# Optimization experiments

Measured on AMD Instinct MI355X. Metric: run time of the kernel, lower is better.

## Reference

```python
import jax, jax.numpy as jnp
import numpy as np

N = 131072          # number of depos
W = 10              # static raster window (cells per dim); covers 2*nsigma*sigma_max/spacing
NSIGMA = 3.0
SQRT2 = 1.4142135623730951


def setup_inputs() -> dict:
    key = jax.random.key(0)
    k1, k2, k3, k4 = jax.random.split(key, 4)
    # Gaussian widths in [0.25, 0.75] (distance units) so +-3 sigma fits in W=10 cells of 0.5
    sigma = 0.25 + 0.5 * jax.random.uniform(k1, (N, 3), dtype=jnp.float32)
    time = 100.0 * jax.random.uniform(k2, (N,), dtype=jnp.float32)
    charge = 5000.0 * jax.random.uniform(k3, (N,), dtype=jnp.float32)
    tail = 50.0 * jax.random.normal(k4, (N, 3), dtype=jnp.float32)
    grid_spacing = jnp.array([0.5, 0.5, 0.5], dtype=jnp.float32)
    return {"sigma": sigma, "time": time, "charge": charge, "tail": tail,
            "grid_spacing": grid_spacing}


def reference(sigma, time, charge, tail, grid_spacing):
    # _transform with pdims=(1,2), tdim=-1: point = [tail[:,1], tail[:,2], time]
    pt = jnp.stack([tail[:, 1], tail[:, 2], time], axis=-1)          # [N,3]
    g = grid_spacing                                                  # [3]
    # window start grid index per depo per dim (nsigma cutoff)
    imin = jnp.floor((pt - NSIGMA * sigma) / g)                       # [N,3]
    # cell edge coordinates for W cells -> W+1 edges
    k = jnp.arange(W + 1, dtype=pt.dtype)                             # [W+1]
    edges = (imin[:, :, None] + k[None, None, :]) * g[None, :, None]  # [N,3,W+1]
    # integrated Gaussian per cell per dim via erf differences
    z = (edges - pt[:, :, None]) / (sigma[:, :, None] * SQRT2)
    cdf = 0.5 * (1.0 + jax.lax.erf(z))
    w = cdf[..., 1:] - cdf[..., :-1]                                  # [N,3,W]
    # separable outer product scaled by charge -> [N,W,W,W]
    rasters = (charge[:, None, None, None]
               * w[:, 0, :, None, None]
               * w[:, 1, None, :, None]
               * w[:, 2, None, None, :])
    offsets = imin.astype(jnp.int32)                                  # [N,3]
    return rasters, offsets
```

## Files before the change

kernel.cpp:

```cpp
#include <hip/hip_runtime.h>
#include <math.h>

#define WAVES_PER_BLOCK 4
#define BLOCK 256

typedef float f32x4 __attribute__((ext_vector_type(4)));
typedef float f32x2 __attribute__((ext_vector_type(2)));

__global__ __launch_bounds__(BLOCK) void raster_kernel(
    const float* __restrict__ sigma,
    const float* __restrict__ time_,
    const float* __restrict__ charge,
    const float* __restrict__ tail,
    const float* __restrict__ gsp,
    float* __restrict__ out_r,
    float* __restrict__ out_off,
    int n, int niter)
{
    __shared__ float s_qw01[WAVES_PER_BLOCK][104];
    __shared__ float s_w2e [WAVES_PER_BLOCK][16];

    const int wave = threadIdx.x >> 6;
    const int lane = threadIdx.x & 63;
    const int nwaves = gridDim.x * WAVES_PER_BLOCK;
    int d = blockIdx.x * WAVES_PER_BLOCK + wave;

    const float g0 = gsp[0], g1 = gsp[1], g2 = gsp[2];

    const int dim = lane / 11;
    const int k   = lane - dim * 11;
    const float gdim = (dim == 0) ? g0 : (dim == 1) ? g1 : g2;

    const int i0a = lane;
    const int s0a = i0a / 10, s1a = 11 + i0a % 10;
    const int i0b = lane + 64;
    const int s0b = i0b / 10, s1b = 11 + i0b % 10;

    int  jc[4], i2c[4];
    bool on[4], cross[4];
    #pragma unroll
    for (int cc = 0; cc < 4; ++cc) {
        int c = lane + 64 * cc;
        on[cc]    = (c < 250);
        int f     = 4 * c;
        jc[cc]    = f / 10;
        i2c[cc]   = f % 10;
        cross[cc] = (i2c[cc] == 8);
    }

    const float* qw  = s_qw01[wave];
    const float* w2e = s_w2e[wave];

    float pt = 0.f, sg = 1.f, q = 0.f;
    if (d < n) {
        if (lane < 33) {
            pt = (dim == 0) ? tail[(size_t)d*3 + 1]
               : (dim == 1) ? tail[(size_t)d*3 + 2]
               : time_[d];
            sg = sigma[(size_t)d*3 + dim];
        }
        q = charge[d];
    }

    for (int it = 0; it < niter; ++it) {
        const bool active = (d < n);
        const int dn = d + nwaves;

        float cdf = 0.0f, iminf = 0.0f;
        if (lane < 33) {
            iminf = floorf((pt - 3.0f * sg) / gdim);
            float edge = (iminf + (float)k) * gdim;
            float z = (edge - pt) / (sg * 1.4142135623730951f);
            cdf = 0.5f * (1.0f + erff(z));
        }
        float cdf1 = __shfl_down(cdf, 1);
        float wv = cdf1 - cdf;

        if (active && lane < 33 && k == 0)
            out_off[(size_t)d*3 + dim] = iminf;

        float npt = 0.f, nsg = 1.f, nq = 0.f;
        if (dn < n) {
            if (lane < 33) {
                npt = (dim == 0) ? tail[(size_t)dn*3 + 1]
                    : (dim == 1) ? tail[(size_t)dn*3 + 2]
                    : time_[dn];
                nsg = sigma[(size_t)dn*3 + dim];
            }
            nq = charge[dn];
        }

        {
            float w0a = __shfl(wv, s0a);
            float w1a = __shfl(wv, s1a);
            s_qw01[wave][i0a] = q * w0a * w1a;
            float w0b = __shfl(wv, s0b);
            float w1b = __shfl(wv, s1b);
            if (i0b < 100) s_qw01[wave][i0b] = q * w0b * w1b;
            if (lane >= 22 && lane < 32) s_w2e[wave][lane - 22] = wv;
            if (lane >= 22 && lane < 25) s_w2e[wave][lane - 22 + 10] = wv;
        }

        if (active) {
            float* base = out_r + (size_t)d * 1000;
            #pragma unroll
            for (int cc = 0; cc < 4; ++cc) {
                if (on[cc]) {
                    float a = qw[jc[cc]];
                    float b = qw[jc[cc] + 1];
                    f32x2 wlo = *reinterpret_cast<const f32x2*>(&w2e[i2c[cc]]);
                    f32x2 whi = *reinterpret_cast<const f32x2*>(&w2e[i2c[cc] + 2]);
                    float qzw = cross[cc] ? b : a;
                    f32x4 v;
                    v.x = a   * wlo.x;
                    v.y = a   * wlo.y;
                    v.z = qzw * whi.x;
                    v.w = qzw * whi.y;
                    *reinterpret_cast<f32x4*>(base + 4 * (lane + 64 * cc)) = v;
                }
            }
        }

        d = dn; pt = npt; sg = nsg; q = nq;
    }
}

extern "C" void kernel_launch(void* const* d_in, const int* in_sizes, int n_in,
                              void* d_out, int out_size, void* d_ws, size_t ws_size,
                              hipStream_t stream) {
    const float* sigma  = (const float*)d_in[0];
    const float* time_  = (const float*)d_in[1];
    const float* charge = (const float*)d_in[2];
    const float* tail   = (const float*)d_in[3];
    const float* gsp    = (const float*)d_in[4];

    const int n = in_sizes[1];
    float* out_r   = (float*)d_out;
    float* out_off = out_r + (size_t)n * 1000;

    const int blocks = 4096;
    const int nwaves = blocks * WAVES_PER_BLOCK;
    const int niter  = (n + nwaves - 1) / nwaves;

    raster_kernel<<<blocks, BLOCK, 0, stream>>>(sigma, time_, charge, tail, gsp,
                                                out_r, out_off, n, niter);
}
```

Measured before the change: 113.7 us.

## Split raster into table-building and store kernels via workspace

```diff
diff --git a/kernel.cpp b/kernel.cpp
--- a/kernel.cpp
+++ b/kernel.cpp
@@ -3,30 +3,23 @@
 
 #define WAVES_PER_BLOCK 4
 #define BLOCK 256
+#define TBL_STRIDE 128
 
 typedef float f32x4 __attribute__((ext_vector_type(4)));
 typedef float f32x2 __attribute__((ext_vector_type(2)));
 
-__global__ __launch_bounds__(BLOCK) void raster_kernel(
-    const float* __restrict__ sigma,
-    const float* __restrict__ time_,
-    const float* __restrict__ charge,
-    const float* __restrict__ tail,
+__global__ __launch_bounds__(BLOCK) void raster_tables(
+    const float* __restrict__ sigma, const float* __restrict__ time_,
+    const float* __restrict__ charge, const float* __restrict__ tail,
     const float* __restrict__ gsp,
-    float* __restrict__ out_r,
-    float* __restrict__ out_off,
-    int n, int niter)
+    float* __restrict__ tbl, float* __restrict__ out_off, int n, int niter)
 {
-    __shared__ float s_qw01[WAVES_PER_BLOCK][104];
-    __shared__ float s_w2e [WAVES_PER_BLOCK][16];
-
     const int wave = threadIdx.x >> 6;
     const int lane = threadIdx.x & 63;
     const int nwaves = gridDim.x * WAVES_PER_BLOCK;
     int d = blockIdx.x * WAVES_PER_BLOCK + wave;
 
     const float g0 = gsp[0], g1 = gsp[1], g2 = gsp[2];
-
     const int dim = lane / 11;
     const int k   = lane - dim * 11;
     const float gdim = (dim == 0) ? g0 : (dim == 1) ? g1 : g2;
@@ -35,6 +28,51 @@
     const int s0a = i0a / 10, s1a = 11 + i0a % 10;
     const int i0b = lane + 64;
     const int s0b = i0b / 10, s1b = 11 + i0b % 10;
+
+    for (int it = 0; it < niter; ++it, d += nwaves) {
+        if (d >= n) break;
+
+        float pt = 0.f, sg = 1.f;
+        if (lane < 33) {
+            pt = (dim == 0) ? tail[(size_t)d*3 + 1]
+               : (dim == 1) ? tail[(size_t)d*3 + 2]
+               : time_[d];
+            sg = sigma[(size_t)d*3 + dim];
+        }
+        float q = charge[d];
+
+        float cdf = 0.f, iminf = 0.f;
+        if (lane < 33) {
+            iminf = floorf((pt - 3.0f * sg) / gdim);
+            float edge = (iminf + (float)k) * gdim;
+            float z = (edge - pt) / (sg * 1.4142135623730951f);
+            cdf = 0.5f * (1.0f + erff(z));
+        }
+        float cdf1 = __shfl_down(cdf, 1);
+        float wv = cdf1 - cdf;
+
+        if (lane < 33 && k == 0)
+            out_off[(size_t)d*3 + dim] = iminf;
+
+        float* t = tbl + (size_t)d * TBL_STRIDE;
+        float w0a = __shfl(wv, s0a), w1a = __shfl(wv, s1a);
+        t[i0a] = q * w0a * w1a;
+        float w0b = __shfl(wv, s0b), w1b = __shfl(wv, s1b);
+        if (i0b < 100) t[i0b] = q * w0b * w1b;
+        if (lane >= 22 && lane < 32) t[104 + lane - 22] = wv;
+        if (lane >= 22 && lane < 25) t[104 + lane - 22 + 10] = wv;
+    }
+}
+
+__global__ __launch_bounds__(BLOCK) void raster_store(
+    const float* __restrict__ tbl, float* __restrict__ out_r, int n, int niter)
+{
+    __shared__ float s_tbl[WAVES_PER_BLOCK][2][120];
+
+    const int wave = threadIdx.x >> 6;
+    const int lane = threadIdx.x & 63;
+    const int nwaves = gridDim.x * WAVES_PER_BLOCK;
+    int d = blockIdx.x * WAVES_PER_BLOCK + wave;
 
     int  jc[4], i2c[4];
     bool on[4], cross[4];
@@ -48,25 +86,103 @@
         cross[cc] = (i2c[cc] == 8);
     }
 
+    f32x4 t0 = {0.f, 0.f, 0.f, 0.f};
+    if (lane < 30 && d < n)
+        t0 = *reinterpret_cast<const f32x4*>(tbl + (size_t)d * TBL_STRIDE + lane * 4);
+    if (lane < 30)
+        *reinterpret_cast<f32x4*>(&s_tbl[wave][0][lane * 4]) = t0;
+
+    for (int it = 0; it < niter; ++it) {
+        const int cur = it & 1;
+        const int dn  = d + nwaves;
+
+        f32x4 tn = {0.f, 0.f, 0.f, 0.f};
+        if (lane < 30 && dn < n)
+            tn = *reinterpret_cast<const f32x4*>(tbl + (size_t)dn * TBL_STRIDE + lane * 4);
+
+        if (d < n) {
+            const float* qw  = s_tbl[wave][cur];
+            const float* w2e = qw + 104;
+            float* base = out_r + (size_t)d * 1000;
+            #pragma unroll
+            for (int cc = 0; cc < 4; ++cc) {
+                if (on[cc]) {
+                    float a = qw[jc[cc]];
+                    float b = qw[jc[cc] + 1];
+                    f32x2 wlo = *reinterpret_cast<const f32x2*>(&w2e[i2c[cc]]);
+                    f32x2 whi = *reinterpret_cast<const f32x2*>(&w2e[i2c[cc] + 2]);
+                    float qzw = cross[cc] ? b : a;
+                    f32x4 v;
+                    v.x = a   * wlo.x;
+                    v.y = a   * wlo.y;
+                    v.z = qzw * whi.x;
+                    v.w = qzw * whi.y;
+                    *reinterpret_cast<f32x4*>(base + 4 * (lane + 64 * cc)) = v;
+                }
+            }
+        }
+
+        if (lane < 30)
+            *reinterpret_cast<f32x4*>(&s_tbl[wave][cur ^ 1][lane * 4]) = tn;
+
+        d = dn;
+    }
+}
+
+__global__ __launch_bounds__(BLOCK) void raster_fused(
+    const float* __restrict__ sigma, const float* __restrict__ time_,
+    const float* __restrict__ charge, const float* __restrict__ tail,
+    const float* __restrict__ gsp,
+    float* __restrict__ out_r, float* __restrict__ out_off, int n, int niter)
+{
+    __shared__ float s_qw01[WAVES_PER_BLOCK][104];
+    __shared__ float s_w2e [WAVES_PER_BLOCK][16];
+
+    const int wave = threadIdx.x >> 6;
+    const int lane = threadIdx.x & 63;
+    const int nwaves = gridDim.x * WAVES_PER_BLOCK;
+    int d = blockIdx.x * WAVES_PER_BLOCK + wave;
+
+    const float g0 = gsp[0], g1 = gsp[1], g2 = gsp[2];
+    const int dim = lane / 11;
+    const int k   = lane - dim * 11;
+    const float gdim = (dim == 0) ? g0 : (dim == 1) ? g1 : g2;
+
+    const int i0a = lane;
+    const int s0a = i0a / 10, s1a = 11 + i0a % 10;
+    const int i0b = lane + 64;
+    const int s0b = i0b / 10, s1b = 11 + i0b % 10;
+
+    int  jc[4], i2c[4];
+    bool on[4], cross[4];
+    #pragma unroll
+    for (int cc = 0; cc < 4; ++cc) {
+        int c = lane + 64 * cc;
+        on[cc]    = (c < 250);
+        int f     = 4 * c;
+        jc[cc]    = f / 10;
+        i2c[cc]   = f % 10;
+        cross[cc] = (i2c[cc] == 8);
+    }
+
     const float* qw  = s_qw01[wave];
     const float* w2e = s_w2e[wave];
 
-    float pt = 0.f, sg = 1.f, q = 0.f;
-    if (d < n) {
-        if (lane < 33) {
-            pt = (dim == 0) ? tail[(size_t)d*3 + 1]
-               : (dim == 1) ? tail[(size_t)d*3 + 2]
-               : time_[d];
-            sg = sigma[(size_t)d*3 + dim];
-        }
-        q = charge[d];
-    }
-
-    for (int it = 0; it < niter; ++it) {
+    for (int it = 0; it < niter; ++it, d += nwaves) {
         const bool active = (d < n);
-        const int dn = d + nwaves;
-
-        float cdf = 0.0f, iminf = 0.0f;
+
+        float pt = 0.f, sg = 1.f, q = 0.f;
+        if (active) {
+            if (lane < 33) {
+                pt = (dim == 0) ? tail[(size_t)d*3 + 1]
+                   : (dim == 1) ? tail[(size_t)d*3 + 2]
+                   : time_[d];
+                sg = sigma[(size_t)d*3 + dim];
+            }
+            q = charge[d];
+        }
+
+        float cdf = 0.f, iminf = 0.f;
         if (lane < 33) {
             iminf = floorf((pt - 3.0f * sg) / gdim);
             float edge = (iminf + (float)k) * gdim;
@@ -79,23 +195,10 @@
         if (active && lane < 33 && k == 0)
             out_off[(size_t)d*3 + dim] = iminf;
 
-        float npt = 0.f, nsg = 1.f, nq = 0.f;
-        if (dn < n) {
-            if (lane < 33) {
-                npt = (dim == 0) ? tail[(size_t)dn*3 + 1]
-                    : (dim == 1) ? tail[(size_t)dn*3 + 2]
-                    : time_[dn];
-                nsg = sigma[(size_t)dn*3 + dim];
-            }
-            nq = charge[dn];
-        }
-
         {
-            float w0a = __shfl(wv, s0a);
-            float w1a = __shfl(wv, s1a);
+            float w0a = __shfl(wv, s0a), w1a = __shfl(wv, s1a);
             s_qw01[wave][i0a] = q * w0a * w1a;
-            float w0b = __shfl(wv, s0b);
-            float w1b = __shfl(wv, s1b);
+            float w0b = __shfl(wv, s0b), w1b = __shfl(wv, s1b);
             if (i0b < 100) s_qw01[wave][i0b] = q * w0b * w1b;
             if (lane >= 22 && lane < 32) s_w2e[wave][lane - 22] = wv;
             if (lane >= 22 && lane < 25) s_w2e[wave][lane - 22 + 10] = wv;
@@ -120,8 +223,6 @@
                 }
             }
         }
-
-        d = dn; pt = npt; sg = nsg; q = nq;
     }
 }
 
@@ -142,6 +243,14 @@
     const int nwaves = blocks * WAVES_PER_BLOCK;
     const int niter  = (n + nwaves - 1) / nwaves;
 
-    raster_kernel<<<blocks, BLOCK, 0, stream>>>(sigma, time_, charge, tail, gsp,
-                                                out_r, out_off, n, niter);
-}
+    const size_t need = (size_t)n * TBL_STRIDE * sizeof(float);
+    if (ws_size >= need) {
+        float* tbl = (float*)d_ws;
+        raster_tables<<<blocks, BLOCK, 0, stream>>>(sigma, time_, charge, tail, gsp,
+                                                    tbl, out_off, n, niter);
+        raster_store <<<blocks, BLOCK, 0, stream>>>(tbl, out_r, n, niter);
+    } else {
+        raster_fused <<<blocks, BLOCK, 0, stream>>>(sigma, time_, charge, tail, gsp,
+                                                    out_r, out_off, n, niter);
+    }
+}
```

Result: slower. 166.7 us (+46.6%).
